# Kernel optimization log

Measured on AMD Instinct MI355X. Metric: run time of the kernel, lower is better.

Reference implementation:

```python
import jax, jax.numpy as jnp
import numpy as np

N = 10000      # nodes
E = 160000     # directed edges (script symmetrizes; random here)
IN = 512       # input feature dim
H = 512        # hidden dim
OUT = 16       # classes


def setup_inputs() -> dict:
    key = jax.random.key(0)
    ks = jax.random.split(key, 8)
    x = jax.random.normal(ks[0], (N, IN), dtype=jnp.float32)
    edge_index = jax.random.randint(ks[1], (2, E), 0, N, dtype=jnp.int64)

    def glorot(k, shape):
        lim = np.sqrt(6.0 / (shape[0] + shape[1])).astype(np.float32)
        return jax.random.uniform(k, shape, dtype=jnp.float32, minval=-lim, maxval=lim)

    W1 = glorot(ks[2], (IN, H));  b1 = jnp.zeros((H,), jnp.float32)
    W2 = glorot(ks[3], (H, H));   b2 = jnp.zeros((H,), jnp.float32)
    Wl = glorot(ks[4], (H, OUT)); bl = jnp.zeros((OUT,), jnp.float32)
    return {"x": x, "edge_index": edge_index,
            "W1": W1, "b1": b1, "W2": W2, "b2": b2, "Wl": Wl, "bl": bl}


def gcn_conv(x, edge_index, W, b):
    """PyG GCNConv: D^{-1/2}(A+I)D^{-1/2} X W + b, unit edge weights."""
    n = x.shape[0]
    src, dst = edge_index[0], edge_index[1]
    h = x @ W                                   # [N, H] transform first (in<=out path)
    # degree with self-loops (all edge weights = 1)
    deg = jnp.zeros((n,), h.dtype).at[dst].add(1.0) + 1.0
    dinv = jax.lax.rsqrt(deg)                   # deg >= 1, no inf handling needed
    norm = dinv[src] * dinv[dst]                # [E]
    msgs = norm[:, None] * h[src]               # [E, H] gather + scale
    agg = jax.ops.segment_sum(msgs, dst, num_segments=n)
    agg = agg + (dinv * dinv)[:, None] * h      # self-loop contribution
    return agg + b


def reference(x, edge_index, W1, b1, W2, b2, Wl, bl):
    h = jax.nn.relu(gcn_conv(x, edge_index, W1, b1))
    # dropout is identity at inference
    h = jax.nn.relu(gcn_conv(h, edge_index, W2, b2))
    return h @ Wl + bl                          # [N, OUT] logits
```

## Files before the change

kernel.cpp:

```cpp
#include <hip/hip_runtime.h>
#include <stdint.h>

#define NF 512
#define OUT_F 16
#define PAD_DEG 64
#define GBM 64
#define GBN 128

typedef __attribute__((ext_vector_type(8))) _Float16 half8;
typedef __attribute__((ext_vector_type(4))) _Float16 half4v;
typedef __attribute__((ext_vector_type(4))) float f32x4;

#define GLOAD_LDS16(g, l) \
  __builtin_amdgcn_global_load_lds((const __attribute__((address_space(1))) unsigned int*)(g), \
                                   (__attribute__((address_space(3))) unsigned int*)(l), 16, 0, 0)


__global__ __launch_bounds__(256) void prep_kernel(
    const float* __restrict__ W1, const float* __restrict__ W2,
    _Float16* __restrict__ T1, _Float16* __restrict__ T2,
    const float* __restrict__ x, _Float16* __restrict__ x16,
    const int* __restrict__ src, const int* __restrict__ dst,
    int* __restrict__ counts, unsigned short* __restrict__ src_pad,
    int E, int Nreal, int Mp) {
    __shared__ float tile[64][65];
    int b = blockIdx.x;
    int xblocks = Mp / 4;

    if (b < 128) {
        int id = b;
        const float* W;  _Float16* WT;
        if (id < 64) { W = W1; WT = T1; }
        else         { W = W2; WT = T2; id -= 64; }
        int k0 = (id & 7) * 64, n0 = (id >> 3) * 64;
        int tr = threadIdx.x >> 4;
        int tc4 = (threadIdx.x & 15) * 4;
#pragma unroll
        for (int i = 0; i < 4; ++i) {
            int r = tr + i * 16;
            float4 v = *(const float4*)(W + (size_t)(k0 + r) * NF + n0 + tc4);
            tile[r][tc4 + 0] = v.x; tile[r][tc4 + 1] = v.y;
            tile[r][tc4 + 2] = v.z; tile[r][tc4 + 3] = v.w;
        }
        __syncthreads();
#pragma unroll
        for (int i = 0; i < 4; ++i) {
            int n = tr + i * 16;
            half4v hv;
#pragma unroll
            for (int j = 0; j < 4; ++j) hv[j] = (_Float16)tile[tc4 + j][n];
            *(half4v*)(WT + (size_t)(n0 + n) * NF + k0 + tc4) = hv;
        }
    } else if (b < 128 + xblocks) {
        int idx = (b - 128) * 256 + threadIdx.x;
        int row = idx >> 6;
        int c8 = (idx & 63) * 8;
        if (row >= Mp) return;
        half8 hv = {0, 0, 0, 0, 0, 0, 0, 0};
        if (row < Nreal) {
            float4 v0 = *(const float4*)(x + (size_t)row * NF + c8);
            float4 v1 = *(const float4*)(x + (size_t)row * NF + c8 + 4);
            hv[0] = (_Float16)v0.x; hv[1] = (_Float16)v0.y;
            hv[2] = (_Float16)v0.z; hv[3] = (_Float16)v0.w;
            hv[4] = (_Float16)v1.x; hv[5] = (_Float16)v1.y;
            hv[6] = (_Float16)v1.z; hv[7] = (_Float16)v1.w;
        }
        *(half8*)(x16 + (size_t)row * NF + c8) = hv;
    } else {
        int e = (b - 128 - xblocks) * 256 + threadIdx.x;
        if (e < E) {
            int d = dst[e];
            int slot = atomicAdd(&counts[d], 1);
            if (slot < PAD_DEG) src_pad[(size_t)d * PAD_DEG + slot] = (unsigned short)src[e];
        }
    }
}


__global__ __launch_bounds__(256) void gemm_mfma_kernel(
    const _Float16* __restrict__ A, const _Float16* __restrict__ BT,
    const int* __restrict__ counts, _Float16* __restrict__ Ch, int nstripes) {
    __shared__ _Float16 lds[2 * (GBM * 64 + GBN * 64)];
    _Float16* As0 = lds;
    _Float16* Bs0 = lds + GBM * 64;
    _Float16* As1 = lds + (GBM * 64 + GBN * 64);
    _Float16* Bs1 = As1 + GBM * 64;

    int b = blockIdx.x;
    int xcd = b & 7;
    int r = b >> 3;
    int s = xcd + 8 * (r >> 2);
    if (s >= nstripes) return;
    int m0 = s * GBM;
    int n0 = (r & 3) * GBN;

    int t = threadIdx.x;
    int w = t >> 6, lane = t & 63, l15 = lane & 15, q = lane >> 4;
    int wr = w >> 1, wc = w & 1;

    int gr = lane >> 3;
    int gc = ((lane & 7) ^ (gr & 7)) * 8;
    const _Float16* Ag0 = A + (size_t)(m0 + w * 8 + gr) * NF + gc;
    const _Float16* Ag1 = A + (size_t)(m0 + 32 + w * 8 + gr) * NF + gc;
    const _Float16* Bg0 = BT + (size_t)(n0 + w * 8 + gr) * NF + gc;
    const _Float16* Bg1 = BT + (size_t)(n0 + 32 + w * 8 + gr) * NF + gc;
    const _Float16* Bg2 = BT + (size_t)(n0 + 64 + w * 8 + gr) * NF + gc;
    const _Float16* Bg3 = BT + (size_t)(n0 + 96 + w * 8 + gr) * NF + gc;

    f32x4 acc[2][4] = {};

    auto stage = [&](_Float16* Asb, _Float16* Bsb, int k0) {
        GLOAD_LDS16(Ag0 + k0, Asb + (w * 8) * 64);
        GLOAD_LDS16(Ag1 + k0, Asb + (32 + w * 8) * 64);
        GLOAD_LDS16(Bg0 + k0, Bsb + (w * 8) * 64);
        GLOAD_LDS16(Bg1 + k0, Bsb + (32 + w * 8) * 64);
        GLOAD_LDS16(Bg2 + k0, Bsb + (64 + w * 8) * 64);
        GLOAD_LDS16(Bg3 + k0, Bsb + (96 + w * 8) * 64);
    };

    auto compute = [&](const _Float16* Asb, const _Float16* Bsb) {
        int key = l15 & 7;
#pragma unroll
        for (int kk = 0; kk < 2; ++kk) {
            int ch = ((kk * 4 + q) ^ key) * 8;
            half8 a[2], bv[4];
#pragma unroll
            for (int rr = 0; rr < 2; ++rr)
                a[rr] = *(const half8*)(Asb + (wr * 32 + rr * 16 + l15) * 64 + ch);
#pragma unroll
            for (int c = 0; c < 4; ++c)
                bv[c] = *(const half8*)(Bsb + (wc * 64 + c * 16 + l15) * 64 + ch);
#pragma unroll
            for (int rr = 0; rr < 2; ++rr)
#pragma unroll
                for (int c = 0; c < 4; ++c)
                    acc[rr][c] = __builtin_amdgcn_mfma_f32_16x16x32_f16(a[rr], bv[c], acc[rr][c], 0, 0, 0);
        }
    };

    stage(As0, Bs0, 0);
#pragma unroll
    for (int kt = 0; kt < NF / 64; kt += 2) {
        __syncthreads();
        if (kt + 1 < NF / 64) stage(As1, Bs1, (kt + 1) * 64);
        compute(As0, Bs0);
        __syncthreads();
        if (kt + 2 < NF / 64) stage(As0, Bs0, (kt + 2) * 64);
        compute(As1, Bs1);
    }

#pragma unroll
    for (int rr = 0; rr < 2; ++rr)
#pragma unroll
        for (int i = 0; i < 4; ++i) {
            int row = m0 + wr * 32 + rr * 16 + q * 4 + i;
            float dv = rsqrtf((float)counts[row] + 1.0f);
#pragma unroll
            for (int c = 0; c < 4; ++c) {
                int col = n0 + wc * 64 + c * 16 + l15;
                Ch[(size_t)row * NF + col] = (_Float16)(acc[rr][c][i] * dv);
            }
        }
}


__global__ __launch_bounds__(256) void agg_kernel(
    const _Float16* __restrict__ hb, const int* __restrict__ counts,
    const unsigned short* __restrict__ src_pad, const float* __restrict__ bias,
    _Float16* __restrict__ out_h, int Mreal) {
    int b = blockIdx.x;
    int slice = b & 7;
    int grp = b >> 3;
    int w = threadIdx.x >> 6, lane = threadIdx.x & 63;
    int node = __builtin_amdgcn_readfirstlane(grp * 4 + w);
    int e8 = lane >> 3, f8 = lane & 7;
    int col = slice * 64 + f8 * 8;

    if (node >= Mreal) {
        if (lane < 8) {
            half8 z = {0, 0, 0, 0, 0, 0, 0, 0};
            *(half8*)(out_h + (size_t)node * NF + col) = z;
        }
        return;
    }

    int cntr = counts[node];
    int cnt = cntr < PAD_DEG ? cntr : PAD_DEG;
    const unsigned short* sp = src_pad + (size_t)node * PAD_DEG;

    float acc[8] = {};
    for (int e = 0; e < cnt; e += 16) {
        half8 v0 = {0, 0, 0, 0, 0, 0, 0, 0};
        half8 v1 = {0, 0, 0, 0, 0, 0, 0, 0};
        int i0 = e + e8, i1 = i0 + 8;
        if (i0 < cnt) {
            int s0 = sp[i0];
            v0 = *(const half8*)(hb + (size_t)s0 * NF + col);
        }
        if (i1 < cnt) {
            int s1 = sp[i1];
            v1 = *(const half8*)(hb + (size_t)s1 * NF + col);
        }
#pragma unroll
        for (int k = 0; k < 8; ++k) acc[k] += (float)v0[k] + (float)v1[k];
    }

    if (e8 == 0) {
        half8 sv = *(const half8*)(hb + (size_t)node * NF + col);
#pragma unroll
        for (int k = 0; k < 8; ++k) acc[k] += (float)sv[k];
    }

#pragma unroll
    for (int m = 8; m <= 32; m <<= 1)
#pragma unroll
        for (int k = 0; k < 8; ++k) acc[k] += __shfl_xor(acc[k], m, 64);

    if (lane < 8) {
        float dv = rsqrtf((float)cntr + 1.0f);
        float4 b0 = *(const float4*)(bias + col);
        float4 b1v = *(const float4*)(bias + col + 4);
        float bb[8] = {b0.x, b0.y, b0.z, b0.w, b1v.x, b1v.y, b1v.z, b1v.w};
        half8 o8;
#pragma unroll
        for (int k = 0; k < 8; ++k)
            o8[k] = (_Float16)fmaxf(fmaf(dv, acc[k], bb[k]), 0.f);
        *(half8*)(out_h + (size_t)node * NF + col) = o8;
    }
}


__global__ __launch_bounds__(256) void head_kernel(
    const _Float16* __restrict__ in, const float* __restrict__ Wl,
    const float* __restrict__ bl, float* __restrict__ out, int M) {
    __shared__ float Ws[NF * OUT_F];
    int tid = threadIdx.x;
    for (int i = tid; i < NF * OUT_F; i += 256) Ws[i] = Wl[i];
    __syncthreads();
    int node = blockIdx.x * 16 + (tid >> 4);
    int o = tid & 15;
    if (node >= M) return;
    const half8* row8 = (const half8*)(in + (size_t)node * NF);
    float acc = 0.f;
#pragma unroll 2
    for (int k8 = 0; k8 < NF / 8; ++k8) {
        half8 hv = row8[k8];
        int kb = k8 * 8;
#pragma unroll
        for (int u = 0; u < 8; ++u)
            acc = fmaf((float)hv[u], Ws[(kb + u) * OUT_F + o], acc);
    }
    out[(size_t)node * OUT_F + o] = acc + bl[o];
}


extern "C" void kernel_launch(void* const* d_in, const int* in_sizes, int n_in,
                              void* d_out, int out_size, void* d_ws, size_t ws_size,
                              hipStream_t stream) {
    const float* x  = (const float*)d_in[0];
    const int* eidx = (const int*)d_in[1];
    const float* W1 = (const float*)d_in[2];
    const float* b1 = (const float*)d_in[3];
    const float* W2 = (const float*)d_in[4];
    const float* b2 = (const float*)d_in[5];
    const float* Wl = (const float*)d_in[6];
    const float* bl = (const float*)d_in[7];

    int N = in_sizes[0] / NF;
    int E = in_sizes[1] / 2;
    int Mp = (N + GBM - 1) & ~(GBM - 1);
    const int* src = eidx;
    const int* dst = eidx + E;

    char* p = (char*)d_ws;
    auto carve = [&](size_t bytes) -> void* {
        void* r = (void*)p;
        p += (bytes + 255) & ~(size_t)255;
        return r;
    };
    _Float16* hbuf = (_Float16*)carve((size_t)Mp * NF * sizeof(_Float16));
    _Float16* abuf = (_Float16*)carve((size_t)Mp * NF * sizeof(_Float16));
    _Float16* W1T  = (_Float16*)carve((size_t)NF * NF * sizeof(_Float16));
    _Float16* W2T  = (_Float16*)carve((size_t)NF * NF * sizeof(_Float16));
    int* counts    = (int*)carve((size_t)Mp * sizeof(int));
    unsigned short* src_pad = (unsigned short*)carve((size_t)N * PAD_DEG * sizeof(unsigned short));

    hipMemsetAsync(counts, 0, (size_t)Mp * sizeof(int), stream);

    int xblocks = Mp / 4;
    int eblocks = (E + 255) / 256;
    prep_kernel<<<dim3(128 + xblocks + eblocks), dim3(256), 0, stream>>>(
        W1, W2, W1T, W2T, x, abuf, src, dst, counts, src_pad, E, N, Mp);

    int nstripes = Mp / GBM;
    int spx = (nstripes + 7) / 8;
    dim3 gg(8 * spx * 4);
    dim3 ga(8 * (Mp / 4));

    gemm_mfma_kernel<<<gg, dim3(256), 0, stream>>>(abuf, W1T, counts, hbuf, nstripes);
    agg_kernel<<<ga, dim3(256), 0, stream>>>(hbuf, counts, src_pad, b1, abuf, N);
    gemm_mfma_kernel<<<gg, dim3(256), 0, stream>>>(abuf, W2T, counts, hbuf, nstripes);
    agg_kernel<<<ga, dim3(256), 0, stream>>>(hbuf, counts, src_pad, b2, abuf, N);
    head_kernel<<<dim3((N + 15) / 16), dim3(256), 0, stream>>>(abuf, Wl, bl, (float*)d_out, N);
}
```

Before: 187.8 us.

## Restructure aggregation: wider column slices, XCD-aware mapping, branchless zero-row gathers

The aggregation kernel now has each wave cover 128 columns with 16 lanes per edge group, so a block's 8 column slices collapse into 4 slices. Blocks are remapped so each XCD pair handles the same slice, which is meant to improve L2 locality of the gathered rows. The self-loop term is folded into the neighbour loop, and out-of-range slots point at an extra zeroed row of hbuf. This removes per-load branches and lets four gathers per lane be issued unconditionally, at the cost of some wasted loads of the zero row and an extra memset.

```diff
diff --git a/kernel.cpp b/kernel.cpp
--- a/kernel.cpp
+++ b/kernel.cpp
@@ -167,19 +167,22 @@
 __global__ __launch_bounds__(256) void agg_kernel(
     const _Float16* __restrict__ hb, const int* __restrict__ counts,
     const unsigned short* __restrict__ src_pad, const float* __restrict__ bias,
-    _Float16* __restrict__ out_h, int Mreal) {
+    _Float16* __restrict__ out_h, int Mreal, int ZR, int nblkTot) {
     int b = blockIdx.x;
-    int slice = b & 7;
-    int grp = b >> 3;
+    int xcd = b & 7, r = b >> 3;
+    int slice = xcd >> 1;
+    int nodeblk = r * 2 + (xcd & 1);
+    if (nodeblk >= nblkTot) return;
     int w = threadIdx.x >> 6, lane = threadIdx.x & 63;
-    int node = __builtin_amdgcn_readfirstlane(grp * 4 + w);
-    int e8 = lane >> 3, f8 = lane & 7;
-    int col = slice * 64 + f8 * 8;
+    int node = __builtin_amdgcn_readfirstlane(nodeblk * 4 + w);
+    int e4 = lane >> 4, f16 = lane & 15;
+    int col = slice * 128 + f16 * 8;
+    size_t obase = (size_t)node * NF + col;
 
     if (node >= Mreal) {
-        if (lane < 8) {
+        if (e4 == 0) {
             half8 z = {0, 0, 0, 0, 0, 0, 0, 0};
-            *(half8*)(out_h + (size_t)node * NF + col) = z;
+            *(half8*)(out_h + obase) = z;
         }
         return;
     }
@@ -187,36 +190,36 @@
     int cntr = counts[node];
     int cnt = cntr < PAD_DEG ? cntr : PAD_DEG;
     const unsigned short* sp = src_pad + (size_t)node * PAD_DEG;
+    int total = cnt + 1;
 
     float acc[8] = {};
-    for (int e = 0; e < cnt; e += 16) {
-        half8 v0 = {0, 0, 0, 0, 0, 0, 0, 0};
-        half8 v1 = {0, 0, 0, 0, 0, 0, 0, 0};
-        int i0 = e + e8, i1 = i0 + 8;
-        if (i0 < cnt) {
-            int s0 = sp[i0];
-            v0 = *(const half8*)(hb + (size_t)s0 * NF + col);
-        }
-        if (i1 < cnt) {
-            int s1 = sp[i1];
-            v1 = *(const half8*)(hb + (size_t)s1 * NF + col);
-        }
-#pragma unroll
-        for (int k = 0; k < 8; ++k) acc[k] += (float)v0[k] + (float)v1[k];
-    }
-
-    if (e8 == 0) {
-        half8 sv = *(const half8*)(hb + (size_t)node * NF + col);
-#pragma unroll
-        for (int k = 0; k < 8; ++k) acc[k] += (float)sv[k];
-    }
-
-#pragma unroll
-    for (int m = 8; m <= 32; m <<= 1)
-#pragma unroll
-        for (int k = 0; k < 8; ++k) acc[k] += __shfl_xor(acc[k], m, 64);
-
-    if (lane < 8) {
+    for (int e = 0; e < total; e += 16) {
+        int sidx[16];
+#pragma unroll
+        for (int i = 0; i < 16; ++i) {
+            int gi = e + i;
+            sidx[i] = gi < cnt ? (int)sp[gi] : (gi == cnt ? node : ZR);
+        }
+        half8 v[4];
+#pragma unroll
+        for (int u = 0; u < 4; ++u) {
+            int s01 = e4 == 0 ? sidx[4 * u + 0] : sidx[4 * u + 1];
+            int s23 = e4 == 2 ? sidx[4 * u + 2] : sidx[4 * u + 3];
+            int s = e4 < 2 ? s01 : s23;
+            v[u] = *(const half8*)(hb + (size_t)s * NF + col);
+        }
+#pragma unroll
+        for (int k = 0; k < 8; ++k)
+            acc[k] += ((float)v[0][k] + (float)v[1][k]) + ((float)v[2][k] + (float)v[3][k]);
+    }
+
+#pragma unroll
+    for (int k = 0; k < 8; ++k) {
+        acc[k] += __shfl_xor(acc[k], 16, 64);
+        acc[k] += __shfl_xor(acc[k], 32, 64);
+    }
+
+    if (e4 == 0) {
         float dv = rsqrtf((float)cntr + 1.0f);
         float4 b0 = *(const float4*)(bias + col);
         float4 b1v = *(const float4*)(bias + col + 4);
@@ -225,7 +228,7 @@
 #pragma unroll
         for (int k = 0; k < 8; ++k)
             o8[k] = (_Float16)fmaxf(fmaf(dv, acc[k], bb[k]), 0.f);
-        *(half8*)(out_h + (size_t)node * NF + col) = o8;
+        *(half8*)(out_h + obase) = o8;
     }
 }
 
@@ -278,7 +281,7 @@
         p += (bytes + 255) & ~(size_t)255;
         return r;
     };
-    _Float16* hbuf = (_Float16*)carve((size_t)Mp * NF * sizeof(_Float16));
+    _Float16* hbuf = (_Float16*)carve((size_t)(Mp + 1) * NF * sizeof(_Float16));
     _Float16* abuf = (_Float16*)carve((size_t)Mp * NF * sizeof(_Float16));
     _Float16* W1T  = (_Float16*)carve((size_t)NF * NF * sizeof(_Float16));
     _Float16* W2T  = (_Float16*)carve((size_t)NF * NF * sizeof(_Float16));
@@ -286,6 +289,7 @@
     unsigned short* src_pad = (unsigned short*)carve((size_t)N * PAD_DEG * sizeof(unsigned short));
 
     hipMemsetAsync(counts, 0, (size_t)Mp * sizeof(int), stream);
+    hipMemsetAsync(hbuf + (size_t)Mp * NF, 0, NF * sizeof(_Float16), stream);
 
     int xblocks = Mp / 4;
     int eblocks = (E + 255) / 256;
@@ -295,11 +299,14 @@
     int nstripes = Mp / GBM;
     int spx = (nstripes + 7) / 8;
     dim3 gg(8 * spx * 4);
-    dim3 ga(8 * (Mp / 4));
+
+    int nblkTot = Mp / 4;
+    int perXcd = (nblkTot + 1) / 2;
+    dim3 ga(8 * perXcd);
 
     gemm_mfma_kernel<<<gg, dim3(256), 0, stream>>>(abuf, W1T, counts, hbuf, nstripes);
-    agg_kernel<<<ga, dim3(256), 0, stream>>>(hbuf, counts, src_pad, b1, abuf, N);
+    agg_kernel<<<ga, dim3(256), 0, stream>>>(hbuf, counts, src_pad, b1, abuf, N, Mp, nblkTot);
     gemm_mfma_kernel<<<gg, dim3(256), 0, stream>>>(abuf, W2T, counts, hbuf, nstripes);
-    agg_kernel<<<ga, dim3(256), 0, stream>>>(hbuf, counts, src_pad, b2, abuf, N);
+    agg_kernel<<<ga, dim3(256), 0, stream>>>(hbuf, counts, src_pad, b2, abuf, N, Mp, nblkTot);
     head_kernel<<<dim3((N + 15) / 16), dim3(256), 0, stream>>>(abuf, Wl, bl, (float*)d_out, N);
 }
```

Result: faster. 171.5 us (-8.6%).
